# Kernel optimization log

Hardware: AMD Instinct MI355X
Metric: run time of the kernel (lower is better)

Reference implementation:

```python
import math
import jax, jax.numpy as jnp
import numpy as np

B, T, D, N = 4, 2048, 1024, 4096  # d_neuron = 4*d_model


def setup_inputs() -> dict:
    key = jax.random.key(0)
    ks = jax.random.split(key, 8)
    s_d = 1.0 / math.sqrt(D)
    s_n = 1.0 / math.sqrt(N)
    return {
        "x": jax.random.normal(ks[0], (B, T, D), jnp.float32),
        "state": jnp.zeros((B, N), jnp.float32),
        "W_main": jax.random.normal(ks[1], (D, N), jnp.float32) * s_d,
        "W_gate": jax.random.normal(ks[2], (D, N), jnp.float32) * s_d,
        "W_mod": jax.random.normal(ks[3], (D, N), jnp.float32) * s_d,
        "W_delta": jax.random.normal(ks[4], (D, N), jnp.float32) * s_d,
        "b_delta": jnp.full((N,), -3.0, jnp.float32),
        "W_out": jax.random.normal(ks[5], (N, D), jnp.float32) * s_n,
        "A_log": jnp.linspace(math.log(0.001), math.log(0.1), N).astype(jnp.float32),
        "sw_logit": jnp.zeros((N,), jnp.float32),  # inv_sigmoid(0.5)
    }


def reference(x, state, W_main, W_gate, W_mod, W_delta, b_delta, W_out, A_log, sw_logit):
    raw = jnp.einsum("btd,dn->btn", x, W_main)            # [B,T,N]
    gate = jax.nn.sigmoid(jnp.einsum("btd,dn->btn", x, W_gate))
    mod = jnp.tanh(jnp.einsum("btd,dn->btn", x, W_mod))
    delta = jax.nn.softplus(jnp.einsum("btd,dn->btn", x, W_delta) + b_delta)
    A = -jnp.exp(A_log)                                    # [N]
    decay = jnp.exp(delta * A)                             # [B,T,N]
    update = (1.0 - decay) * gate * jnp.tanh(raw)

    # linear recurrence h_t = decay_t * h_{t-1} + update_t via associative scan
    def combine(c, n):
        a1, b1 = c
        a2, b2 = n
        return a1 * a2, a2 * b1 + b2

    a_cum, b_cum = jax.lax.associative_scan(combine, (decay, update), axis=1)
    all_states = a_cum * state[:, None, :] + b_cum         # [B,T,N]
    final_state = all_states[:, -1]

    sw = jax.nn.sigmoid(sw_logit)
    mixed = (1.0 - sw) * jax.nn.gelu(raw, approximate=False) + sw * all_states
    output = mixed * (1.0 + mod)                           # dropout=0 (eval)
    output = jnp.einsum("btn,nd->btd", output, W_out)
    return output, final_state
```

## Files before the change

kernel.cpp:

```cpp
#include <hip/hip_runtime.h>
#include <math.h>
#include <stdint.h>

#define BB  4
#define TT  2048
#define DD  1024
#define NNq 4096
#define BT  (BB*TT)
#define NCH 32
#define TCH (TT/NCH)

typedef _Float16 f16;
typedef __attribute__((ext_vector_type(8))) _Float16 half8;
typedef __attribute__((ext_vector_type(4))) _Float16 half4;
typedef __attribute__((ext_vector_type(2))) _Float16 half2v;
typedef __attribute__((ext_vector_type(4))) float f32x4;

__device__ __forceinline__ float sigmoid_f(float x){ return 1.f/(1.f+__expf(-x)); }
__device__ __forceinline__ float tanh_f(float x){
  float cx = fminf(fmaxf(x,-15.f),15.f);
  float e  = __expf(2.f*cx);
  return (e-1.f)/(e+1.f);
}
__device__ __forceinline__ float softplus_f(float x){
  return (x>15.f)? x : __logf(1.f+__expf(x));
}

__device__ __forceinline__ void gld_lds16(const void* g, void* l){
  __builtin_amdgcn_global_load_lds(
      (const __attribute__((address_space(1))) void*)(uintptr_t)g,
      (__attribute__((address_space(3))) void*)(uintptr_t)l,
      16, 0, 0);
}

__global__ __launch_bounds__(256) void cast_f16_k(const float* __restrict__ src,
                                                  f16* __restrict__ dst){
  size_t i = ((size_t)blockIdx.x*256 + threadIdx.x)*4;
  float4 v = *(const float4*)(src + i);
  union { f16 h[4]; uint2 u; } o;
  o.h[0]=(f16)v.x; o.h[1]=(f16)v.y; o.h[2]=(f16)v.z; o.h[3]=(f16)v.w;
  *(uint2*)(dst + i) = o.u;
}

__global__ __launch_bounds__(256) void transpose_cast_k(const float* __restrict__ src,
                                                        f16* __restrict__ dst,
                                                        int R, int C){
  __shared__ float tile[32][33];
  int c0 = blockIdx.x*32, r0 = blockIdx.y*32;
  int tx = threadIdx.x, ty = threadIdx.y;
  #pragma unroll
  for (int i=0;i<4;i++){ int r = ty + i*8; tile[r][tx] = src[(size_t)(r0+r)*C + c0+tx]; }
  __syncthreads();
  #pragma unroll
  for (int i=0;i<4;i++){ int c = ty + i*8; dst[(size_t)(c0+c)*R + r0+tx] = (f16)tile[tx][c]; }
}

template<int OUT_F32>
__global__ __launch_bounds__(256)
void gemm_bt(const f16* __restrict__ A, int lda,
             const f16* __restrict__ Bt, int ldb,
             void* __restrict__ Cout, int ldc, int K)
{
  __shared__ f16 lsA[128*64];
  __shared__ f16 lsB[128*64];
  const int tid  = threadIdx.x;
  const int lane = tid & 63;
  const int wave = tid >> 6;
  const int wm = wave >> 1, wn = wave & 1;

  const int gx   = gridDim.x;
  const int nwg  = gx * gridDim.y;
  const int orig = blockIdx.y * gx + blockIdx.x;
  const int cpx  = nwg >> 3;
  const int lgc  = (orig & 7) * cpx + (orig >> 3);
  const int m0   = (lgc / gx) * 128;
  const int n0   = (lgc % gx) * 128;

  const f16* Ag = A  + (size_t)m0 * lda;
  const f16* Bg = Bt + (size_t)n0 * ldb;

  f32x4 acc[4][4] = {};

  for (int k0 = 0; k0 < K; k0 += 64) {
    __syncthreads();
    #pragma unroll
    for (int i = 0; i < 4; i++) {
      const int j   = i*256 + tid;
      const int row = j >> 3;
      const int ce  = (j & 7) * 8;
      gld_lds16(Ag + (size_t)row*lda + k0 + ce, &lsA[j*8]);
      gld_lds16(Bg + (size_t)row*ldb + k0 + ce, &lsB[j*8]);
    }
    __syncthreads();
    #pragma unroll
    for (int ks = 0; ks < 2; ks++) {
      const int kk = ks*32 + (lane>>4)*8;
      half8 af[4], bfr[4];
      #pragma unroll
      for (int mi=0; mi<4; mi++)
        af[mi] = *(const half8*)&lsA[(wm*64 + mi*16 + (lane&15))*64 + kk];
      #pragma unroll
      for (int ni=0; ni<4; ni++)
        bfr[ni] = *(const half8*)&lsB[(wn*64 + ni*16 + (lane&15))*64 + kk];
      #pragma unroll
      for (int mi=0; mi<4; mi++)
        #pragma unroll
        for (int ni=0; ni<4; ni++)
          acc[mi][ni] = __builtin_amdgcn_mfma_f32_16x16x32_f16(af[mi], bfr[ni], acc[mi][ni], 0, 0, 0);
    }
  }

  const int crow = m0 + wm*64 + (lane>>4)*4;
  const int ccol = n0 + wn*64 + (lane&15);
  #pragma unroll
  for (int mi=0; mi<4; mi++)
    #pragma unroll
    for (int ni=0; ni<4; ni++)
      #pragma unroll
      for (int r=0; r<4; r++) {
        size_t idx = (size_t)(crow + mi*16 + r) * ldc + (ccol + ni*16);
        if (OUT_F32) ((float*)Cout)[idx] = acc[mi][ni][r];
        else         ((f16*)Cout)[idx]   = (f16)acc[mi][ni][r];
      }
}

template<int VEC>
__global__ __launch_bounds__(256) void scan_agg_v(
    const f16* __restrict__ zg, const f16* __restrict__ zr, const f16* __restrict__ zd,
    const float* __restrict__ Alog, const float* __restrict__ bdelta,
    float* __restrict__ AggA, float* __restrict__ AggB, int NC)
{
  typedef __attribute__((ext_vector_type(VEC))) _Float16 hv;
  const int nb = NC / (256*VEC);
  const int bx = blockIdx.x;
  const int nl = ((bx % nb)*256 + threadIdx.x)*VEC;
  const int c  = (bx / nb) % NCH;
  const int b  = bx / (nb*NCH);
  float An[VEC], bd[VEC], pA[VEC], pB[VEC];
  #pragma unroll
  for (int v=0;v<VEC;v++){
    An[v] = -__expf(Alog[nl+v]); bd[v] = bdelta[nl+v]; pA[v]=1.f; pB[v]=0.f;
  }
  const size_t rbase = (size_t)(b*TT + c*TCH);
  #pragma unroll 4
  for (int t=0; t<TCH; ++t) {
    size_t rr = rbase + t;
    hv hg = *(const hv*)(zg + rr*NC + nl);
    hv hr = *(const hv*)(zr + rr*(size_t)NNq + nl);
    hv hd = *(const hv*)(zd + rr*NC + nl);
    #pragma unroll
    for (int v=0;v<VEC;v++){
      float g  = (float)hg[v];
      float r  = (float)hr[v];
      float dz = (float)hd[v] + bd[v];
      float d  = __expf(An[v] * softplus_f(dz));
      float u  = (1.f-d) * sigmoid_f(g) * tanh_f(r);
      pA[v] *= d;
      pB[v] = fmaf(d, pB[v], u);
    }
  }
  size_t o = ((size_t)(b*NCH + c))*NNq + nl;
  #pragma unroll
  for (int v=0;v<VEC;v++){ AggA[o+v]=pA[v]; AggB[o+v]=pB[v]; }
}

__global__ __launch_bounds__(256) void scan_agg_k(
    const f16* __restrict__ zg, const f16* __restrict__ zr, const f16* __restrict__ zd,
    const float* __restrict__ Alog, const float* __restrict__ bdelta,
    float* __restrict__ AggA, float* __restrict__ AggB, int NC)
{
  const int nb = NC >> 8;
  const int bx = blockIdx.x;
  const int nl = (bx % nb)*256 + threadIdx.x;
  const int c  = (bx / nb) % NCH;
  const int b  = bx / (nb*NCH);
  const float An = -__expf(Alog[nl]);
  const float bd = bdelta[nl];
  float pA = 1.f, pB = 0.f;
  const size_t rbase = (size_t)(b*TT + c*TCH);
  #pragma unroll 4
  for (int t=0; t<TCH; ++t) {
    size_t rr = rbase + t;
    float g  = (float)zg[rr*NC  + nl];
    float r  = (float)zr[rr*(size_t)NNq + nl];
    float dz = (float)zd[rr*NC  + nl] + bd;
    float d  = __expf(An * softplus_f(dz));
    float u  = (1.f-d) * sigmoid_f(g) * tanh_f(r);
    pA *= d;
    pB = fmaf(d, pB, u);
  }
  size_t o = ((size_t)(b*NCH + c))*NNq + nl;
  AggA[o] = pA;
  AggB[o] = pB;
}

__global__ __launch_bounds__(256) void scan_mid_k(
    const float* __restrict__ AggA, const float* __restrict__ AggB,
    const float* __restrict__ state0, float* __restrict__ sIn,
    float* __restrict__ fstate, int NC)
{
  int gi = blockIdx.x*256 + threadIdx.x;
  int b  = gi / NC, nl = gi % NC;
  float s = state0[(size_t)b*NNq + nl];
  #pragma unroll
  for (int c=0; c<NCH; ++c) {
    size_t o = ((size_t)(b*NCH + c))*NNq + nl;
    sIn[o] = s;
    s = fmaf(AggA[o], s, AggB[o]);
  }
  fstate[(size_t)b*NNq + nl] = s;
}

template<int VEC>
__global__ __launch_bounds__(256) void scan_apply_v(
    const f16* zr, const f16* __restrict__ zg, const f16* __restrict__ zm,
    const f16* __restrict__ zd,
    const float* __restrict__ Alog, const float* __restrict__ bdelta,
    const float* __restrict__ swl, const float* __restrict__ sIn,
    f16* P, int NC)
{
  typedef __attribute__((ext_vector_type(VEC))) _Float16 hv;
  const int nb = NC / (256*VEC);
  const int bx = blockIdx.x;
  const int nl = ((bx % nb)*256 + threadIdx.x)*VEC;
  const int c  = (bx / nb) % NCH;
  const int b  = bx / (nb*NCH);
  float An[VEC], bd[VEC], sw[VEC], s[VEC];
  #pragma unroll
  for (int v=0;v<VEC;v++){
    An[v] = -__expf(Alog[nl+v]); bd[v] = bdelta[nl+v];
    sw[v] = sigmoid_f(swl[nl+v]);
    s[v]  = sIn[((size_t)(b*NCH + c))*NNq + nl + v];
  }
  const size_t rbase = (size_t)(b*TT + c*TCH);
  for (int t=0; t<TCH; ++t) {
    size_t rr = rbase + t;
    hv hr = *(const hv*)(zr + rr*(size_t)NNq + nl);
    hv hg = *(const hv*)(zg + rr*NC + nl);
    hv hm = *(const hv*)(zm + rr*NC + nl);
    hv hd = *(const hv*)(zd + rr*NC + nl);
    hv ho;
    #pragma unroll
    for (int v=0;v<VEC;v++){
      float r  = (float)hr[v];
      float g  = (float)hg[v];
      float m  = (float)hm[v];
      float dz = (float)hd[v] + bd[v];
      float d  = __expf(An[v] * softplus_f(dz));
      float u  = (1.f-d) * sigmoid_f(g) * tanh_f(r);
      s[v] = fmaf(d, s[v], u);
      float gel = 0.5f*r*(1.f+erff(r*0.70710678118654752f));
      float mod = tanh_f(m);
      ho[v] = (f16)(((1.f-sw[v])*gel + sw[v]*s[v])*(1.f+mod));
    }
    *(hv*)(P + rr*(size_t)NNq + nl) = ho;
  }
}

__global__ __launch_bounds__(256) void scan_apply_k(
    const f16* zr, const f16* __restrict__ zg, const f16* __restrict__ zm,
    const f16* __restrict__ zd,
    const float* __restrict__ Alog, const float* __restrict__ bdelta,
    const float* __restrict__ swl, const float* __restrict__ sIn,
    f16* P, int NC)
{
  const int nb = NC >> 8;
  const int bx = blockIdx.x;
  const int nl = (bx % nb)*256 + threadIdx.x;
  const int c  = (bx / nb) % NCH;
  const int b  = bx / (nb*NCH);
  const float An = -__expf(Alog[nl]);
  const float bd = bdelta[nl];
  const float sw = sigmoid_f(swl[nl]);
  float s = sIn[((size_t)(b*NCH + c))*NNq + nl];
  const size_t rbase = (size_t)(b*TT + c*TCH);
  for (int t=0; t<TCH; ++t) {
    size_t rr = rbase + t;
    float r  = (float)zr[rr*(size_t)NNq + nl];
    float g  = (float)zg[rr*NC  + nl];
    float m  = (float)zm[rr*NC  + nl];
    float dz = (float)zd[rr*NC  + nl] + bd;
    float d  = __expf(An * softplus_f(dz));
    float u  = (1.f-d) * sigmoid_f(g) * tanh_f(r);
    s = fmaf(d, s, u);
    float gel = 0.5f*r*(1.f+erff(r*0.70710678118654752f));
    float mod = tanh_f(m);
    P[rr*(size_t)NNq + nl] = (f16)(((1.f-sw)*gel + sw*s)*(1.f+mod));
  }
}

extern "C" void kernel_launch(void* const* d_in, const int* in_sizes, int n_in,
                              void* d_out, int out_size, void* d_ws, size_t ws_size,
                              hipStream_t stream)
{
  const float* x      = (const float*)d_in[0];
  const float* state0 = (const float*)d_in[1];
  const float* Wmain  = (const float*)d_in[2];
  const float* Wgate  = (const float*)d_in[3];
  const float* Wmod   = (const float*)d_in[4];
  const float* Wdelta = (const float*)d_in[5];
  const float* bdelta = (const float*)d_in[6];
  const float* Wout   = (const float*)d_in[7];
  const float* Alog   = (const float*)d_in[8];
  const float* swl    = (const float*)d_in[9];

  auto al = [](size_t v)->size_t { return (v + 255) & ~(size_t)255; };
  const size_t sz_xb  = al((size_t)BT*DD*2);
  const size_t sz_wt  = al((size_t)NNq*DD*2);
  const size_t sz_wto = al((size_t)DD*NNq*2);
  const size_t sz_P   = al((size_t)BT*NNq*2);
  const size_t sz_agg = al((size_t)BB*NCH*NNq*4);
  const size_t fixed  = sz_xb + 4*sz_wt + sz_wto + sz_P + 3*sz_agg;

  int NCC = 16;
  {
    const int cand[5] = {1,2,4,8,16};
    for (int i=0;i<5;i++){
      size_t zchunk = al((size_t)BT*(NNq/cand[i])*2);
      if (fixed + 3*zchunk <= ws_size) { NCC = cand[i]; break; }
    }
  }
  const int NC = NNq / NCC;
  const size_t sz_z = al((size_t)BT*NC*2);

  char* ws = (char*)d_ws;
  size_t off = 0;
  auto alloc = [&](size_t bytes)->void* { void* p = ws + off; off += bytes; return p; };
  f16*   xb   = (f16*)alloc(sz_xb);
  f16*   wt0  = (f16*)alloc(sz_wt);
  f16*   wt1  = (f16*)alloc(sz_wt);
  f16*   wt2  = (f16*)alloc(sz_wt);
  f16*   wt3  = (f16*)alloc(sz_wt);
  f16*   wto  = (f16*)alloc(sz_wto);
  f16*   P    = (f16*)alloc(sz_P);
  float* AggA = (float*)alloc(sz_agg);
  float* AggB = (float*)alloc(sz_agg);
  float* sIn  = (float*)alloc(sz_agg);
  f16*   z1   = (f16*)alloc(sz_z);
  f16*   z2   = (f16*)alloc(sz_z);
  f16*   z3   = (f16*)alloc(sz_z);

  float* fstate = (float*)d_out + (size_t)BT*DD;

  cast_f16_k<<<(BT*DD)/1024, 256, 0, stream>>>(x, xb);
  transpose_cast_k<<<dim3(NNq/32, DD/32), dim3(32,8), 0, stream>>>(Wmain,  wt0, DD, NNq);
  transpose_cast_k<<<dim3(NNq/32, DD/32), dim3(32,8), 0, stream>>>(Wgate,  wt1, DD, NNq);
  transpose_cast_k<<<dim3(NNq/32, DD/32), dim3(32,8), 0, stream>>>(Wmod,   wt2, DD, NNq);
  transpose_cast_k<<<dim3(NNq/32, DD/32), dim3(32,8), 0, stream>>>(Wdelta, wt3, DD, NNq);
  transpose_cast_k<<<dim3(DD/32, NNq/32), dim3(32,8), 0, stream>>>(Wout,   wto, NNq, DD);

  const int VEC = (NC >= 2048) ? 4 : ((NC >= 512) ? 2 : 1);
  const dim3 gz(NC/128, BT/128);
  for (int cc = 0; cc < NCC; ++cc) {
    const int n0 = cc * NC;
    gemm_bt<0><<<gz, 256, 0, stream>>>(xb, DD, wt0 + (size_t)n0*DD, DD, P + n0, NNq, DD);
    gemm_bt<0><<<gz, 256, 0, stream>>>(xb, DD, wt1 + (size_t)n0*DD, DD, z1, NC, DD);
    gemm_bt<0><<<gz, 256, 0, stream>>>(xb, DD, wt2 + (size_t)n0*DD, DD, z2, NC, DD);
    gemm_bt<0><<<gz, 256, 0, stream>>>(xb, DD, wt3 + (size_t)n0*DD, DD, z3, NC, DD);

    if (VEC == 4) {
      scan_agg_v<4><<<BB*NCH*(NC/1024), 256, 0, stream>>>(z1, P + n0, z3,
          Alog + n0, bdelta + n0, AggA + n0, AggB + n0, NC);
    } else if (VEC == 2) {
      scan_agg_v<2><<<BB*NCH*(NC/512), 256, 0, stream>>>(z1, P + n0, z3,
          Alog + n0, bdelta + n0, AggA + n0, AggB + n0, NC);
    } else {
      scan_agg_k<<<BB*NCH*(NC/256), 256, 0, stream>>>(z1, P + n0, z3,
          Alog + n0, bdelta + n0, AggA + n0, AggB + n0, NC);
    }

    scan_mid_k<<<(BB*NC)/256, 256, 0, stream>>>(AggA + n0, AggB + n0,
        state0 + n0, sIn + n0, fstate + n0, NC);

    if (VEC == 4) {
      scan_apply_v<4><<<BB*NCH*(NC/1024), 256, 0, stream>>>(P + n0, z1, z2, z3,
          Alog + n0, bdelta + n0, swl + n0, sIn + n0, P + n0, NC);
    } else if (VEC == 2) {
      scan_apply_v<2><<<BB*NCH*(NC/512), 256, 0, stream>>>(P + n0, z1, z2, z3,
          Alog + n0, bdelta + n0, swl + n0, sIn + n0, P + n0, NC);
    } else {
      scan_apply_k<<<BB*NCH*(NC/256), 256, 0, stream>>>(P + n0, z1, z2, z3,
          Alog + n0, bdelta + n0, swl + n0, sIn + n0, P + n0, NC);
    }
  }

  gemm_bt<1><<<dim3(DD/128, BT/128), 256, 0, stream>>>(P, NNq, wto, NNq, d_out, DD, NNq);
}
```

Before: 1.005 ms.

## Batch four projection GEMMs into one launch and split-K the output GEMM

The four per-chunk projection GEMMs are merged into a single launch that uses blockIdx.z to pick the weight matrix and destination. This relies on the transposed weights and z buffers being contiguous in the workspace. The output GEMM is split along K into two halves that accumulate into a pre-zeroed fp32 output with atomicAdd, doubling the number of workgroups for the small 1024-wide output. This adds a zeroing pass and atomic traffic, and makes the fp32 summation order nondeterministic.

```diff
diff --git a/kernel.cpp b/kernel.cpp
--- a/kernel.cpp
+++ b/kernel.cpp
@@ -9,11 +9,10 @@
 #define BT  (BB*TT)
 #define NCH 32
 #define TCH (TT/NCH)
+#define SPLITK 2
 
 typedef _Float16 f16;
 typedef __attribute__((ext_vector_type(8))) _Float16 half8;
-typedef __attribute__((ext_vector_type(4))) _Float16 half4;
-typedef __attribute__((ext_vector_type(2))) _Float16 half2v;
 typedef __attribute__((ext_vector_type(4))) float f32x4;
 
 __device__ __forceinline__ float sigmoid_f(float x){ return 1.f/(1.f+__expf(-x)); }
@@ -31,6 +30,11 @@
       (const __attribute__((address_space(1))) void*)(uintptr_t)g,
       (__attribute__((address_space(3))) void*)(uintptr_t)l,
       16, 0, 0);
+}
+
+__global__ __launch_bounds__(256) void zero_f32_k(float* __restrict__ p){
+  size_t i = ((size_t)blockIdx.x*256 + threadIdx.x)*4;
+  *(float4*)(p + i) = make_float4(0.f,0.f,0.f,0.f);
 }
 
 __global__ __launch_bounds__(256) void cast_f16_k(const float* __restrict__ src,
@@ -55,33 +59,21 @@
   for (int i=0;i<4;i++){ int c = ty + i*8; dst[(size_t)(c0+c)*R + r0+tx] = (f16)tile[tx][c]; }
 }
 
-template<int OUT_F32>
-__global__ __launch_bounds__(256)
-void gemm_bt(const f16* __restrict__ A, int lda,
-             const f16* __restrict__ Bt, int ldb,
-             void* __restrict__ Cout, int ldc, int K)
-{
-  __shared__ f16 lsA[128*64];
-  __shared__ f16 lsB[128*64];
+struct TileOut { int crow, ccol; };
+__device__ __forceinline__ TileOut gemm_tile_body(
+    const f16* __restrict__ A, int lda, const f16* __restrict__ Bt, int ldb,
+    int m0, int n0, int kbeg, int Klen,
+    f16* lsA, f16* lsB, f32x4 (*acc)[4])
+{
   const int tid  = threadIdx.x;
   const int lane = tid & 63;
   const int wave = tid >> 6;
   const int wm = wave >> 1, wn = wave & 1;
 
-  const int gx   = gridDim.x;
-  const int nwg  = gx * gridDim.y;
-  const int orig = blockIdx.y * gx + blockIdx.x;
-  const int cpx  = nwg >> 3;
-  const int lgc  = (orig & 7) * cpx + (orig >> 3);
-  const int m0   = (lgc / gx) * 128;
-  const int n0   = (lgc % gx) * 128;
-
-  const f16* Ag = A  + (size_t)m0 * lda;
-  const f16* Bg = Bt + (size_t)n0 * ldb;
-
-  f32x4 acc[4][4] = {};
-
-  for (int k0 = 0; k0 < K; k0 += 64) {
+  const f16* Ag = A  + (size_t)m0 * lda + kbeg;
+  const f16* Bg = Bt + (size_t)n0 * ldb + kbeg;
+
+  for (int k0 = 0; k0 < Klen; k0 += 64) {
     __syncthreads();
     #pragma unroll
     for (int i = 0; i < 4; i++) {
@@ -109,19 +101,71 @@
           acc[mi][ni] = __builtin_amdgcn_mfma_f32_16x16x32_f16(af[mi], bfr[ni], acc[mi][ni], 0, 0, 0);
     }
   }
-
-  const int crow = m0 + wm*64 + (lane>>4)*4;
-  const int ccol = n0 + wn*64 + (lane&15);
+  TileOut o;
+  o.crow = m0 + wm*64 + (lane>>4)*4;
+  o.ccol = n0 + wn*64 + (lane&15);
+  return o;
+}
+
+__device__ __forceinline__ void xcd_tile(int &m0, int &n0){
+  const int gx   = gridDim.x;
+  const int nwg  = gx * gridDim.y;
+  const int orig = blockIdx.y * gx + blockIdx.x;
+  const int cpx  = nwg >> 3;
+  const int lgc  = (orig & 7) * cpx + (orig >> 3);
+  m0 = (lgc / gx) * 128;
+  n0 = (lgc % gx) * 128;
+}
+
+__global__ __launch_bounds__(256)
+void gemm_proj4(const f16* __restrict__ A, int lda,
+                const f16* __restrict__ wtbase, size_t wstride,
+                f16* __restrict__ dst0, int ldc0,
+                f16* __restrict__ dstz, size_t zstride, int ldcz, int K)
+{
+  __shared__ f16 lsA[128*64];
+  __shared__ f16 lsB[128*64];
+  int m0, n0; xcd_tile(m0, n0);
+  const int z = blockIdx.z;
+  const f16* Bt = wtbase + (size_t)z * wstride;
+  f16* dst; int ldc;
+  if (z == 0) { dst = dst0; ldc = ldc0; }
+  else        { dst = dstz + (size_t)(z-1)*zstride; ldc = ldcz; }
+
+  f32x4 acc[4][4] = {};
+  TileOut t = gemm_tile_body(A, lda, Bt, K , m0, n0, 0, K, lsA, lsB, acc);
+
   #pragma unroll
   for (int mi=0; mi<4; mi++)
     #pragma unroll
     for (int ni=0; ni<4; ni++)
       #pragma unroll
-      for (int r=0; r<4; r++) {
-        size_t idx = (size_t)(crow + mi*16 + r) * ldc + (ccol + ni*16);
-        if (OUT_F32) ((float*)Cout)[idx] = acc[mi][ni][r];
-        else         ((f16*)Cout)[idx]   = (f16)acc[mi][ni][r];
-      }
+      for (int r=0; r<4; r++)
+        dst[(size_t)(t.crow + mi*16 + r) * ldc + (t.ccol + ni*16)] = (f16)acc[mi][ni][r];
+}
+
+__global__ __launch_bounds__(256)
+void gemm_out_sk(const f16* __restrict__ A, int lda,
+                 const f16* __restrict__ Bt, int ldb,
+                 float* __restrict__ Cout, int ldc, int K)
+{
+  __shared__ f16 lsA[128*64];
+  __shared__ f16 lsB[128*64];
+  int m0, n0; xcd_tile(m0, n0);
+  const int kc   = K / SPLITK;
+  const int kbeg = blockIdx.z * kc;
+
+  f32x4 acc[4][4] = {};
+  TileOut t = gemm_tile_body(A, lda, Bt, ldb, m0, n0, kbeg, kc, lsA, lsB, acc);
+
+  #pragma unroll
+  for (int mi=0; mi<4; mi++)
+    #pragma unroll
+    for (int ni=0; ni<4; ni++)
+      #pragma unroll
+      for (int r=0; r<4; r++)
+        atomicAdd(&Cout[(size_t)(t.crow + mi*16 + r) * ldc + (t.ccol + ni*16)],
+                  acc[mi][ni][r]);
 }
 
 template<int VEC>
@@ -342,6 +386,8 @@
 
   float* fstate = (float*)d_out + (size_t)BT*DD;
 
+  zero_f32_k<<<(BT*DD)/1024, 256, 0, stream>>>((float*)d_out);
+
   cast_f16_k<<<(BT*DD)/1024, 256, 0, stream>>>(x, xb);
   transpose_cast_k<<<dim3(NNq/32, DD/32), dim3(32,8), 0, stream>>>(Wmain,  wt0, DD, NNq);
   transpose_cast_k<<<dim3(NNq/32, DD/32), dim3(32,8), 0, stream>>>(Wgate,  wt1, DD, NNq);
@@ -350,13 +396,11 @@
   transpose_cast_k<<<dim3(DD/32, NNq/32), dim3(32,8), 0, stream>>>(Wout,   wto, NNq, DD);
 
   const int VEC = (NC >= 2048) ? 4 : ((NC >= 512) ? 2 : 1);
-  const dim3 gz(NC/128, BT/128);
   for (int cc = 0; cc < NCC; ++cc) {
     const int n0 = cc * NC;
-    gemm_bt<0><<<gz, 256, 0, stream>>>(xb, DD, wt0 + (size_t)n0*DD, DD, P + n0, NNq, DD);
-    gemm_bt<0><<<gz, 256, 0, stream>>>(xb, DD, wt1 + (size_t)n0*DD, DD, z1, NC, DD);
-    gemm_bt<0><<<gz, 256, 0, stream>>>(xb, DD, wt2 + (size_t)n0*DD, DD, z2, NC, DD);
-    gemm_bt<0><<<gz, 256, 0, stream>>>(xb, DD, wt3 + (size_t)n0*DD, DD, z3, NC, DD);
+    gemm_proj4<<<dim3(NC/128, BT/128, 4), 256, 0, stream>>>(
+        xb, DD, wt0 + (size_t)n0*DD, sz_wt/2,
+        P + n0, NNq, z1, sz_z/2, NC, DD);
 
     if (VEC == 4) {
       scan_agg_v<4><<<BB*NCH*(NC/1024), 256, 0, stream>>>(z1, P + n0, z3,
@@ -384,5 +428,6 @@
     }
   }
 
-  gemm_bt<1><<<dim3(DD/128, BT/128), 256, 0, stream>>>(P, NNq, wto, NNq, d_out, DD, NNq);
-}
+  gemm_out_sk<<<dim3(DD/128, BT/128, SPLITK), 256, 0, stream>>>(
+      P, NNq, wto, NNq, (float*)d_out, DD, NNq);
+}
```

Measured after the change: 1.011 ms. No clear change (+0.6%).
